# Optimization experiments

Hardware: AMD Instinct MI355X
Metric: run time of the kernel (lower is better)

Reference implementation:

```python
import jax, jax.numpy as jnp
import numpy as np

B, S, C = 4, 256, 128
H, W = 512, 512

def setup_inputs() -> dict:
    key = jax.random.key(0)
    k1, k2 = jax.random.split(key)
    graph_lstm_output = jax.random.normal(k1, (B, S, C), dtype=jnp.float32)
    # SLIC segment ids are 1-based: values in [1, max_segments]
    slic_output = jax.random.randint(k2, (B, H, W), 1, S + 1, dtype=jnp.int32)
    return {"graph_lstm_output": graph_lstm_output, "slic_output": slic_output}

def reference(graph_lstm_output, slic_output):
    # Original loop accumulates graph_lstm_output[:, cycle, :] wherever
    # slic_output - 1 == cycle; since ids are unique per pixel this is exactly
    # a per-pixel gather: out[b,h,w,:] = graph_lstm_output[b, slic[b,h,w]-1, :].
    b, h, w = slic_output.shape
    idx = (slic_output - 1).reshape(b, h * w, 1)          # [B, H*W, 1], 0-based
    out = jnp.take_along_axis(graph_lstm_output, idx, axis=1)  # [B, H*W, C]
    return out.reshape(b, h, w, graph_lstm_output.shape[-1])
```

## Files before the change

### kernel.cpp

```cpp
#include <hip/hip_runtime.h>


typedef float f32x4 __attribute__((ext_vector_type(4)));

constexpr int C4      = 32;
constexpr int LOG_C4  = 5;
constexpr int LOG_HW  = 18;
constexpr int LOG_S   = 8;
constexpr int UNROLL  = 4;
constexpr int BLK     = 256;

__global__ __launch_bounds__(BLK)
void convert2image_kernel(const f32x4* __restrict__ lstm,
                          const int*   __restrict__ slic,
                          f32x4*       __restrict__ out,
                          int n4)
{
    int base = blockIdx.x * (BLK * UNROLL) + threadIdx.x;

    int  src[UNROLL];
    bool ok [UNROLL];

    #pragma unroll
    for (int u = 0; u < UNROLL; ++u) {
        int i = base + u * BLK;
        ok[u] = (i < n4);
        if (ok[u]) {
            int c4  = i & (C4 - 1);
            int pix = i >> LOG_C4;
            int b   = pix >> LOG_HW;
            int seg = slic[pix] - 1;
            src[u]  = (((b << LOG_S) + seg) << LOG_C4) + c4;
        }
    }

    #pragma unroll
    for (int u = 0; u < UNROLL; ++u) {
        if (ok[u]) {
            f32x4 v = lstm[src[u]];
            __builtin_nontemporal_store(v, &out[base + u * BLK]);
        }
    }
}

extern "C" void kernel_launch(void* const* d_in, const int* in_sizes, int n_in,
                              void* d_out, int out_size, void* d_ws, size_t ws_size,
                              hipStream_t stream) {
    const f32x4* lstm = (const f32x4*)d_in[0];
    const int*   slic = (const int*)d_in[1];
    f32x4*       out  = (f32x4*)d_out;

    int n4 = out_size / 4;
    int blocks = (n4 + BLK * UNROLL - 1) / (BLK * UNROLL);
    convert2image_kernel<<<blocks, BLK, 0, stream>>>(lstm, slic, out, n4);
}
```

Before: 542.7 us.

## Use persistent grid-stride blocks with software-prefetched segment ids

Replaces the one-tile-per-block launch with a grid capped at 2048 persistent blocks. Each block loops over tiles and loads the next tile's segment ids while the current tile's gathers and stores are in flight. Unroll grows from 4 to 8, and a remainder path in block 0 handles leftover elements. The aim is to hide the slic-load to gather dependency latency and cut block launch overhead, at the cost of more registers and fewer resident blocks per CU.

```diff
diff --git a/kernel.cpp b/kernel.cpp
--- a/kernel.cpp
+++ b/kernel.cpp
@@ -3,12 +3,15 @@
 
 typedef float f32x4 __attribute__((ext_vector_type(4)));
 
-constexpr int C4      = 32;
-constexpr int LOG_C4  = 5;
-constexpr int LOG_HW  = 18;
-constexpr int LOG_S   = 8;
-constexpr int UNROLL  = 4;
-constexpr int BLK     = 256;
+constexpr int C4       = 32;
+constexpr int LOG_C4   = 5;
+constexpr int LOG_HW   = 18;
+constexpr int LOG_S    = 8;
+constexpr int UNROLL   = 8;
+constexpr int BLK      = 256;
+constexpr int TILE     = BLK * UNROLL;
+constexpr int LOG_TILE = 11;
+constexpr int MAXGRID  = 2048;
 
 __global__ __launch_bounds__(BLK)
 void convert2image_kernel(const f32x4* __restrict__ lstm,
@@ -16,29 +19,72 @@
                           f32x4*       __restrict__ out,
                           int n4)
 {
-    int base = blockIdx.x * (BLK * UNROLL) + threadIdx.x;
+    const int n_tiles = n4 >> LOG_TILE;
+    const int t       = threadIdx.x;
 
-    int  src[UNROLL];
-    bool ok [UNROLL];
+    if ((int)blockIdx.x < n_tiles) {
+        int tile   = blockIdx.x;
+        int stride = gridDim.x;
+        int base   = tile * TILE + t;
 
-    #pragma unroll
-    for (int u = 0; u < UNROLL; ++u) {
-        int i = base + u * BLK;
-        ok[u] = (i < n4);
-        if (ok[u]) {
+        int src[UNROLL];
+        {
+            int sg[UNROLL];
+            #pragma unroll
+            for (int u = 0; u < UNROLL; ++u)
+                sg[u] = slic[(base + u * BLK) >> LOG_C4];
+            #pragma unroll
+            for (int u = 0; u < UNROLL; ++u) {
+                int i  = base + u * BLK;
+                int c4 = i & (C4 - 1);
+                int b  = i >> (LOG_C4 + LOG_HW);
+                src[u] = (((b << LOG_S) + (sg[u] - 1)) << LOG_C4) + c4;
+            }
+        }
+
+        for (;;) {
+            const int  next  = tile + stride;
+            const bool more  = next < n_tiles;
+            const int  nbase = next * TILE + t;
+
+            f32x4 v[UNROLL];
+            #pragma unroll
+            for (int u = 0; u < UNROLL; ++u)
+                v[u] = lstm[src[u]];
+
+            int nsg[UNROLL];
+            if (more) {
+                #pragma unroll
+                for (int u = 0; u < UNROLL; ++u)
+                    nsg[u] = slic[(nbase + u * BLK) >> LOG_C4];
+            }
+
+            #pragma unroll
+            for (int u = 0; u < UNROLL; ++u)
+                __builtin_nontemporal_store(v[u], &out[base + u * BLK]);
+
+            if (!more) break;
+
+            #pragma unroll
+            for (int u = 0; u < UNROLL; ++u) {
+                int i  = nbase + u * BLK;
+                int c4 = i & (C4 - 1);
+                int b  = i >> (LOG_C4 + LOG_HW);
+                src[u] = (((b << LOG_S) + (nsg[u] - 1)) << LOG_C4) + c4;
+            }
+            base = nbase;
+            tile = next;
+        }
+    }
+
+    if (blockIdx.x == 0) {
+        for (int i = (n_tiles << LOG_TILE) + t; i < n4; i += BLK) {
             int c4  = i & (C4 - 1);
             int pix = i >> LOG_C4;
             int b   = pix >> LOG_HW;
             int seg = slic[pix] - 1;
-            src[u]  = (((b << LOG_S) + seg) << LOG_C4) + c4;
-        }
-    }
-
-    #pragma unroll
-    for (int u = 0; u < UNROLL; ++u) {
-        if (ok[u]) {
-            f32x4 v = lstm[src[u]];
-            __builtin_nontemporal_store(v, &out[base + u * BLK]);
+            f32x4 vv = lstm[(((b << LOG_S) + seg) << LOG_C4) + c4];
+            __builtin_nontemporal_store(vv, &out[i]);
         }
     }
 }
@@ -50,7 +96,8 @@
     const int*   slic = (const int*)d_in[1];
     f32x4*       out  = (f32x4*)d_out;
 
-    int n4 = out_size / 4;
-    int blocks = (n4 + BLK * UNROLL - 1) / (BLK * UNROLL);
+    int n4      = out_size / 4;
+    int n_tiles = n4 >> LOG_TILE;
+    int blocks  = n_tiles < MAXGRID ? (n_tiles > 0 ? n_tiles : 1) : MAXGRID;
     convert2image_kernel<<<blocks, BLK, 0, stream>>>(lstm, slic, out, n4);
 }
```

Result: faster. 520.1 us (-4.2%).
